# Kernel tuning notes

Measured on AMD Instinct MI355X. Metric: run time of the kernel, lower is better.

## Reference

```python
import jax, jax.numpy as jnp
import numpy as np

B, S, D_IN, D_OUT = 8, 2048, 1024, 1024

def setup_inputs() -> dict:
    key = jax.random.key(0)
    k1, k2, k3, k4 = jax.random.split(key, 4)
    sc = 0.02
    return {
        "x": jax.random.normal(k1, (B, S, D_IN), dtype=jnp.float32),
        "Wq": jax.random.normal(k2, (D_IN, D_OUT), dtype=jnp.float32) * sc,
        "Wk": jax.random.normal(k3, (D_IN, D_OUT), dtype=jnp.float32) * sc,
        "Wv": jax.random.normal(k4, (D_IN, D_OUT), dtype=jnp.float32) * sc,
    }

def reference(x, Wq, Wk, Wv):
    b, n, _ = x.shape
    d_out = Wq.shape[1]
    q = jnp.einsum('bsd,de->bse', x, Wq)   # [b, n, d_out]
    k = jnp.einsum('bsd,de->bse', x, Wk)
    v = jnp.einsum('bsd,de->bse', x, Wv)
    scores = jnp.einsum('bie,bje->bij', q, k)  # [b, n, n]
    # causal mask: positions j > i set to -inf (triu, diagonal=1)
    causal = jnp.triu(jnp.ones((n, n), dtype=bool), k=1)
    scores = jnp.where(causal[None, :, :], -jnp.inf, scores)
    # NOTE: source applies softmax over dim=1 (query axis), scaled by sqrt(d_out)
    weights = jax.nn.softmax(scores / jnp.sqrt(jnp.float32(d_out)), axis=1)
    # dropout is identity in eval mode (p=0)
    return jnp.einsum('bij,bje->bie', weights, v)
```

## Files before the change

kernel.cpp:

```cpp
#include <hip/hip_runtime.h>
#include <hip/hip_bf16.h>


using bf16 = __hip_bfloat16;
typedef __attribute__((ext_vector_type(8))) short short8;
typedef __attribute__((ext_vector_type(4))) float f32x4;

__device__ __forceinline__ float bfbits2f(unsigned short u) {
  return __uint_as_float((unsigned)u << 16);
}

__global__ void cvt_kernel(const float* __restrict__ in, bf16* __restrict__ out) {
  size_t i = ((size_t)blockIdx.x * 256 + threadIdx.x) * 4;
  float4 v = *(const float4*)(in + i);
  alignas(8) bf16 h[4] = {__float2bfloat16(v.x), __float2bfloat16(v.y),
                          __float2bfloat16(v.z), __float2bfloat16(v.w)};
  *(unsigned long long*)(out + i) = *(const unsigned long long*)h;
}

__global__ void pre_kernel(const float* __restrict__ x,
                           const float* __restrict__ W0, const float* __restrict__ W1,
                           const float* __restrict__ W2, bf16* __restrict__ Wt,
                           float* __restrict__ lbuf, bf16* __restrict__ Xb) {
  int tid = threadIdx.x;
  int zz = blockIdx.z;
  if (zz == 3) {
    int bid = blockIdx.y * 16 + blockIdx.x;
    if (bid < 64) lbuf[bid * 256 + tid] = 0.f;
    return;
  }
  if (zz >= 4) {
    size_t cb = (size_t)(zz - 4) * 256 + blockIdx.y * 16 + blockIdx.x;
    size_t i = (cb * 256 + tid) * 4;
    float4 v = *(const float4*)(x + i);
    alignas(8) bf16 h[4] = {__float2bfloat16(v.x), __float2bfloat16(v.y),
                            __float2bfloat16(v.z), __float2bfloat16(v.w)};
    *(unsigned long long*)(Xb + i) = *(const unsigned long long*)h;
    return;
  }
  const float* W = zz == 0 ? W0 : zz == 1 ? W1 : W2;
  bf16* O = Wt + (size_t)zz * 1048576ull;
  __shared__ float t[64][65];
  int n0 = blockIdx.x * 64, k0 = blockIdx.y * 64;
#pragma unroll
  for (int i = 0; i < 4; ++i) {
    int idx = i * 1024 + tid * 4;
    int r = idx >> 6, c = idx & 63;
    float4 v = *(const float4*)(W + (size_t)(k0 + r) * 1024 + n0 + c);
    t[r][c] = v.x; t[r][c + 1] = v.y; t[r][c + 2] = v.z; t[r][c + 3] = v.w;
  }
  __syncthreads();
#pragma unroll
  for (int i = 0; i < 4; ++i) {
    int idx = i * 1024 + tid * 4;
    int r = idx >> 6, c = idx & 63;
    alignas(8) bf16 h[4] = {__float2bfloat16(t[c][r]), __float2bfloat16(t[c + 1][r]),
                            __float2bfloat16(t[c + 2][r]), __float2bfloat16(t[c + 3][r])};
    *(unsigned long long*)(O + (size_t)(n0 + r) * 1024 + k0 + c) = *(const unsigned long long*)h;
  }
}

__global__ void vhat_kernel(const bf16* __restrict__ QKV, const float* __restrict__ l,
                            bf16* __restrict__ Vt) {
  int lb = blockIdx.z;
  const unsigned short* V =
      (const unsigned short*)QKV + ((size_t)lb * 3 + 2) * 2097152ull;
  bf16* O = Vt + (size_t)lb * 2097152ull;
  const float* lc = l + lb * 2048;
  __shared__ float t[64][65];
  __shared__ float rl[64];
  int j0 = blockIdx.x * 64, e0 = blockIdx.y * 64;
  int tid = threadIdx.x;
  if (tid < 64) rl[tid] = 1.0f / lc[j0 + tid];
#pragma unroll
  for (int i = 0; i < 4; ++i) {
    int idx = i * 1024 + tid * 4;
    int r = idx >> 6, c = idx & 63;
    ushort4 u = *(const ushort4*)(V + (size_t)(j0 + r) * 1024 + e0 + c);
    t[r][c] = bfbits2f(u.x); t[r][c + 1] = bfbits2f(u.y);
    t[r][c + 2] = bfbits2f(u.z); t[r][c + 3] = bfbits2f(u.w);
  }
  __syncthreads();
#pragma unroll
  for (int i = 0; i < 4; ++i) {
    int idx = i * 1024 + tid * 4;
    int r = idx >> 6, c = idx & 63;
    alignas(8) bf16 h[4] = {
        __float2bfloat16(t[c][r] * rl[c]), __float2bfloat16(t[c + 1][r] * rl[c + 1]),
        __float2bfloat16(t[c + 2][r] * rl[c + 2]), __float2bfloat16(t[c + 3][r] * rl[c + 3])};
    *(unsigned long long*)(O + (size_t)(e0 + r) * 2048 + j0 + c) = *(const unsigned long long*)h;
  }
}

template <int EPI, bool TRI>
__device__ __forceinline__ void gemm_bt_body(
    const bf16* __restrict__ A, const bf16* __restrict__ B, void* __restrict__ Cv,
    int lda, int ldb, int ldc, int Kin, int zdivA, int zmodB,
    unsigned long long sA, unsigned long long sB, unsigned long long sC,
    float* __restrict__ lptr) {
  unsigned bz, bx, by;
  if constexpr (TRI) {
    const unsigned gx = gridDim.x;
    const unsigned total = gx * gridDim.z;
    unsigned id = blockIdx.x + gx * blockIdx.z;
    unsigned lid = (id & 7) * (total >> 3) + (id >> 3);
    bz = lid / gx;
    unsigned t = lid - bz * gx;
    int r = (int)((__builtin_sqrtf(8.f * (float)t + 1.f) - 1.f) * 0.5f);
    while ((r + 1) * (r + 2) / 2 <= (int)t) ++r;
    while (r * (r + 1) / 2 > (int)t) --r;
    by = (unsigned)r;
    bx = t - (unsigned)(r * (r + 1) / 2);
  } else {
    const unsigned gx = gridDim.x, gy = gridDim.y;
    const unsigned per_z = gx * gy;
    const unsigned total = per_z * gridDim.z;
    unsigned id = blockIdx.x + gx * (blockIdx.y + gy * blockIdx.z);
    unsigned lid = (id & 7) * (total >> 3) + (id >> 3);
    bz = lid / per_z;
    unsigned rem = lid - bz * per_z;
    constexpr unsigned H = 8;
    const unsigned band = rem / (gx * H);
    const unsigned w = rem - band * (gx * H);
    bx = w / H;
    by = band * H + (w - bx * H);
  }

  const int z = (int)bz;
  A += (unsigned long long)(z / zdivA) * sA;
  B += (unsigned long long)(z % zmodB) * sB;
  const int K = Kin;

  alignas(16) __shared__ bf16 As[128 * 64];
  alignas(16) __shared__ bf16 Bs[128 * 64];

  const int tid = threadIdx.x, wave = tid >> 6, lane = tid & 63;
  const int m0 = by * 128, n0 = bx * 128;
  const int srow = tid >> 3;
  const int scol_g = ((tid & 7) ^ (srow & 7)) * 8;
  const int scol_l = (tid & 7) * 8;
  const int wm = (wave >> 1) * 64, wn = (wave & 1) * 64;
  const int fm = lane & 15, sw = lane & 7, kg = lane >> 4;

  f32x4 acc[4][4];
#pragma unroll
  for (int mi = 0; mi < 4; ++mi)
#pragma unroll
    for (int ni = 0; ni < 4; ++ni) acc[mi][ni] = (f32x4){0.f, 0.f, 0.f, 0.f};

  const bf16* Arow = A + (size_t)m0 * lda;
  const bf16* Brow = B + (size_t)n0 * ldb;

  for (int k0 = 0; k0 < K; k0 += 64) {
    __syncthreads();
#pragma unroll
    for (int c = 0; c < 4; ++c) {
      int row = c * 32 + srow;
      __builtin_amdgcn_global_load_lds(
          (const __attribute__((address_space(1))) void*)(Arow + (size_t)row * lda + k0 + scol_g),
          (__attribute__((address_space(3))) void*)(As + row * 64 + scol_l), 16, 0, 0);
    }
#pragma unroll
    for (int c = 0; c < 4; ++c) {
      int row = c * 32 + srow;
      __builtin_amdgcn_global_load_lds(
          (const __attribute__((address_space(1))) void*)(Brow + (size_t)row * ldb + k0 + scol_g),
          (__attribute__((address_space(3))) void*)(Bs + row * 64 + scol_l), 16, 0, 0);
    }
    __syncthreads();
#pragma unroll
    for (int ks = 0; ks < 2; ++ks) {
      const int pc = ((ks * 4 + kg) ^ sw) * 8;
      short8 af[4], bf_[4];
#pragma unroll
      for (int i = 0; i < 4; ++i) {
        af[i] = *(const short8*)(As + (wm + i * 16 + fm) * 64 + pc);
        bf_[i] = *(const short8*)(Bs + (wn + i * 16 + fm) * 64 + pc);
      }
#pragma unroll
      for (int mi = 0; mi < 4; ++mi)
#pragma unroll
        for (int ni = 0; ni < 4; ++ni)
          acc[mi][ni] = __builtin_amdgcn_mfma_f32_16x16x32_bf16(af[mi], bf_[ni], acc[mi][ni], 0, 0, 0);
    }
  }

  const int cr = kg * 4, cc = fm;
  if constexpr (EPI == 0) {
    bf16* C = (bf16*)Cv + (unsigned long long)z * sC;
#pragma unroll
    for (int mi = 0; mi < 4; ++mi)
#pragma unroll
      for (int ni = 0; ni < 4; ++ni)
#pragma unroll
        for (int r = 0; r < 4; ++r)
          C[(size_t)(m0 + wm + mi * 16 + cr + r) * ldc + (n0 + wn + ni * 16 + cc)] =
              __float2bfloat16(acc[mi][ni][r]);
  } else {
    bf16* C = (bf16*)Cv + (unsigned long long)z * sC;
    float colpart[4] = {0.f, 0.f, 0.f, 0.f};
#pragma unroll
    for (int mi = 0; mi < 4; ++mi)
#pragma unroll
      for (int ni = 0; ni < 4; ++ni)
#pragma unroll
        for (int r = 0; r < 4; ++r) {
          int gm = m0 + wm + mi * 16 + cr + r;
          int gn = n0 + wn + ni * 16 + cc;
          float s = acc[mi][ni][r] * 0.03125f;
          float p = (gn <= gm) ? __expf(s) : 0.f;
          colpart[ni] += p;
          C[(size_t)gm * ldc + gn] = __float2bfloat16(p);
        }
    float* lcol = lptr + (size_t)z * 2048 + n0 + wn;
#pragma unroll
    for (int ni = 0; ni < 4; ++ni) {
      float s = colpart[ni];
      s += __shfl_xor(s, 16);
      s += __shfl_xor(s, 32);
      if (lane < 16) atomicAdd(&lcol[ni * 16 + lane], s);
    }
  }
}

__global__ __launch_bounds__(256, 4) void gemm_qkv(
    const bf16* __restrict__ A, const bf16* __restrict__ B, void* __restrict__ Cv,
    int lda, int ldb, int ldc, int Kin, int zdivA, int zmodB,
    unsigned long long sA, unsigned long long sB, unsigned long long sC) {
  gemm_bt_body<0, false>(A, B, Cv, lda, ldb, ldc, Kin, zdivA, zmodB, sA, sB, sC, nullptr);
}
__global__ __launch_bounds__(256, 4) void gemm_scores(
    const bf16* __restrict__ A, const bf16* __restrict__ B, void* __restrict__ Cv,
    int lda, int ldb, int ldc, int Kin, int zdivA, int zmodB,
    unsigned long long sA, unsigned long long sB, unsigned long long sC,
    float* __restrict__ lptr) {
  gemm_bt_body<1, true>(A, B, Cv, lda, ldb, ldc, Kin, zdivA, zmodB, sA, sB, sC, lptr);
}

__global__ __launch_bounds__(256, 4) void gemm_pv(
    const bf16* __restrict__ Pm, const bf16* __restrict__ Vt, float* __restrict__ out,
    unsigned long long sA, unsigned long long sB, unsigned long long sC) {
  const unsigned gx = gridDim.x, gy = gridDim.y;
  const unsigned per_z = gx * gy;
  const unsigned total = per_z * gridDim.z;
  unsigned id = blockIdx.x + gx * (blockIdx.y + gy * blockIdx.z);
  unsigned lid = (id & 7) * (total >> 3) + (id >> 3);
  const unsigned bz = lid / per_z;
  unsigned rem = lid - bz * per_z;
  const unsigned bx = rem >> 3;
  const unsigned pp = rem & 7;
  const int z = (int)bz;

  const bf16* A = Pm + (unsigned long long)z * sA;
  const bf16* B = Vt + (unsigned long long)z * sB;
  float* C = out + (unsigned long long)z * sC;

  alignas(16) __shared__ bf16 As[128 * 64];
  alignas(16) __shared__ bf16 Bs[128 * 64];

  const int tid = threadIdx.x, wave = tid >> 6, lane = tid & 63;
  const int srow = tid >> 3;
  const int scol_g = ((tid & 7) ^ (srow & 7)) * 8;
  const int scol_l = (tid & 7) * 8;
  const int wm = (wave >> 1) * 64, wn = (wave & 1) * 64;
  const int fm = lane & 15, sw = lane & 7, kg = lane >> 4;
  const int n0 = (int)bx * 128;
  const bf16* Brow = B + (size_t)n0 * 2048;

  auto phase = [&](int by, int K) {
    const int m0 = by * 128;
    const bf16* Arow = A + (size_t)m0 * 2048;
    f32x4 acc[4][4];
#pragma unroll
    for (int mi = 0; mi < 4; ++mi)
#pragma unroll
      for (int ni = 0; ni < 4; ++ni) acc[mi][ni] = (f32x4){0.f, 0.f, 0.f, 0.f};

    for (int k0 = 0; k0 < K; k0 += 64) {
      __syncthreads();
#pragma unroll
      for (int c = 0; c < 4; ++c) {
        int row = c * 32 + srow;
        __builtin_amdgcn_global_load_lds(
            (const __attribute__((address_space(1))) void*)(Arow + (size_t)row * 2048 + k0 + scol_g),
            (__attribute__((address_space(3))) void*)(As + row * 64 + scol_l), 16, 0, 0);
      }
#pragma unroll
      for (int c = 0; c < 4; ++c) {
        int row = c * 32 + srow;
        __builtin_amdgcn_global_load_lds(
            (const __attribute__((address_space(1))) void*)(Brow + (size_t)row * 2048 + k0 + scol_g),
            (__attribute__((address_space(3))) void*)(Bs + row * 64 + scol_l), 16, 0, 0);
      }
      __syncthreads();
#pragma unroll
      for (int ks = 0; ks < 2; ++ks) {
        const int pc = ((ks * 4 + kg) ^ sw) * 8;
        short8 af[4], bf_[4];
#pragma unroll
        for (int i = 0; i < 4; ++i) {
          af[i] = *(const short8*)(As + (wm + i * 16 + fm) * 64 + pc);
          bf_[i] = *(const short8*)(Bs + (wn + i * 16 + fm) * 64 + pc);
        }
#pragma unroll
        for (int mi = 0; mi < 4; ++mi)
#pragma unroll
          for (int ni = 0; ni < 4; ++ni)
            acc[mi][ni] = __builtin_amdgcn_mfma_f32_16x16x32_bf16(af[mi], bf_[ni], acc[mi][ni], 0, 0, 0);
      }
    }
    const int cr = kg * 4, cc = fm;
#pragma unroll
    for (int mi = 0; mi < 4; ++mi)
#pragma unroll
      for (int ni = 0; ni < 4; ++ni)
#pragma unroll
        for (int r = 0; r < 4; ++r)
          C[(size_t)(m0 + wm + mi * 16 + cr + r) * 1024 + (n0 + wn + ni * 16 + cc)] =
              acc[mi][ni][r];
  };

  phase(15 - (int)pp, (16 - (int)pp) * 128);
  phase((int)pp, ((int)pp + 1) * 128);
}

extern "C" void kernel_launch(void* const* d_in, const int* in_sizes, int n_in,
                              void* d_out, int out_size, void* d_ws, size_t ws_size,
                              hipStream_t stream) {
  const float* x = (const float*)d_in[0];
  const float* Wq = (const float*)d_in[1];
  const float* Wk = (const float*)d_in[2];
  const float* Wv = (const float*)d_in[3];
  float* out = (float*)d_out;

  constexpr unsigned long long X_EL = 2048ull * 1024;
  constexpr unsigned long long QKV_EL = 3ull * X_EL;
  constexpr unsigned long long P_EL = 2048ull * 2048;
  constexpr unsigned long long VT_EL = 1024ull * 2048;
  constexpr unsigned long long WT_B = 3ull * 1024 * 1024 * 2;
  constexpr unsigned long long LB_B = 8ull * 2048 * 4;
  constexpr unsigned long long PER_B = 2 * (X_EL + QKV_EL + P_EL + VT_EL);

  size_t NB = 1;
  for (size_t nb : {(size_t)8, (size_t)4, (size_t)2})
    if (WT_B + LB_B + nb * PER_B <= ws_size) { NB = nb; break; }

  char* p = (char*)d_ws;
  bf16* Wt = (bf16*)p;   p += WT_B;
  float* lbuf = (float*)p; p += LB_B;
  bf16* Xb = (bf16*)p;   p += 2 * NB * X_EL;
  bf16* QKV = (bf16*)p;  p += 2 * NB * QKV_EL;
  bf16* P = (bf16*)p;    p += 2 * NB * P_EL;
  bf16* Vt = (bf16*)p;

  pre_kernel<<<dim3(16, 16, (unsigned)(4 + NB * 8)), 256, 0, stream>>>(
      x, Wq, Wk, Wv, Wt, lbuf, Xb);

  for (size_t b0 = 0; b0 < 8; b0 += NB) {
    if (b0)
      cvt_kernel<<<dim3((unsigned)(NB * 2048)), 256, 0, stream>>>(x + b0 * X_EL, Xb);
    gemm_qkv<<<dim3(8, 16, (unsigned)(NB * 3)), 256, 0, stream>>>(
        Xb, Wt, QKV, 1024, 1024, 1024, 1024, 3, 3, X_EL, 1048576ull, X_EL);
    gemm_scores<<<dim3(136, 1, (unsigned)NB), 256, 0, stream>>>(
        QKV, QKV + X_EL, P, 1024, 1024, 2048, 1024, 1, 1 << 30, QKV_EL, QKV_EL, P_EL,
        lbuf + b0 * 2048);
    vhat_kernel<<<dim3(32, 16, (unsigned)NB), 256, 0, stream>>>(QKV, lbuf + b0 * 2048, Vt);
    gemm_pv<<<dim3(8, 8, (unsigned)NB), 256, 0, stream>>>(
        P, Vt, out + b0 * X_EL, P_EL, VT_EL, X_EL);
  }
}
```

Baseline: 327.1 us.

## Split causal PV GEMM into equal K-chunks across blocks with atomic partial sums

The PV GEMM previously paired row-tiles (15-p, p) per block to balance the causal triangle. Now the triangle's 136 K-steps per column tile are split into 16 equal 17-step segments. Each block handles one segment, possibly crossing row-tile boundaries, and writes full tiles directly or partial tiles via float atomicAdd. This doubles the grid to improve occupancy and balance, but it adds a memset of the output and atomic traffic on partial tiles.

```diff
diff --git a/kernel.cpp b/kernel.cpp
--- a/kernel.cpp
+++ b/kernel.cpp
@@ -5,6 +5,7 @@
 using bf16 = __hip_bfloat16;
 typedef __attribute__((ext_vector_type(8))) short short8;
 typedef __attribute__((ext_vector_type(4))) float f32x4;
+typedef unsigned long long ull;
 
 __device__ __forceinline__ float bfbits2f(unsigned short u) {
   return __uint_as_float((unsigned)u << 16);
@@ -247,8 +248,8 @@
   unsigned lid = (id & 7) * (total >> 3) + (id >> 3);
   const unsigned bz = lid / per_z;
   unsigned rem = lid - bz * per_z;
-  const unsigned bx = rem >> 3;
-  const unsigned pp = rem & 7;
+  const unsigned bx = rem >> 4;
+  const unsigned q = rem & 15;
   const int z = (int)bz;
 
   const bf16* A = Pm + (unsigned long long)z * sA;
@@ -266,17 +267,29 @@
   const int fm = lane & 15, sw = lane & 7, kg = lane >> 4;
   const int n0 = (int)bx * 128;
   const bf16* Brow = B + (size_t)n0 * 2048;
-
-  auto phase = [&](int by, int K) {
+  const int cr = kg * 4, cc = fm;
+
+  const int s0 = (int)q * 17, s1 = s0 + 17;
+  int by = 0;
+  while ((by + 1) * (by + 2) <= s0) ++by;
+  int cur = s0;
+
+  while (cur < s1) {
+    const int Cprev = by * (by + 1);
+    const int Cend = (by + 1) * (by + 2);
+    const int b = s1 < Cend ? s1 : Cend;
+    const int kbeg = (cur - Cprev) * 64, kend = (b - Cprev) * 64;
+    const bool full = (cur == Cprev) && (b == Cend);
     const int m0 = by * 128;
     const bf16* Arow = A + (size_t)m0 * 2048;
+
     f32x4 acc[4][4];
 #pragma unroll
     for (int mi = 0; mi < 4; ++mi)
 #pragma unroll
       for (int ni = 0; ni < 4; ++ni) acc[mi][ni] = (f32x4){0.f, 0.f, 0.f, 0.f};
 
-    for (int k0 = 0; k0 < K; k0 += 64) {
+    for (int k0 = kbeg; k0 < kend; k0 += 64) {
       __syncthreads();
 #pragma unroll
       for (int c = 0; c < 4; ++c) {
@@ -309,19 +322,29 @@
             acc[mi][ni] = __builtin_amdgcn_mfma_f32_16x16x32_bf16(af[mi], bf_[ni], acc[mi][ni], 0, 0, 0);
       }
     }
-    const int cr = kg * 4, cc = fm;
-#pragma unroll
-    for (int mi = 0; mi < 4; ++mi)
-#pragma unroll
-      for (int ni = 0; ni < 4; ++ni)
-#pragma unroll
-        for (int r = 0; r < 4; ++r)
-          C[(size_t)(m0 + wm + mi * 16 + cr + r) * 1024 + (n0 + wn + ni * 16 + cc)] =
-              acc[mi][ni][r];
-  };
-
-  phase(15 - (int)pp, (16 - (int)pp) * 128);
-  phase((int)pp, ((int)pp + 1) * 128);
+
+    if (full) {
+#pragma unroll
+      for (int mi = 0; mi < 4; ++mi)
+#pragma unroll
+        for (int ni = 0; ni < 4; ++ni)
+#pragma unroll
+          for (int r = 0; r < 4; ++r)
+            C[(size_t)(m0 + wm + mi * 16 + cr + r) * 1024 + (n0 + wn + ni * 16 + cc)] =
+                acc[mi][ni][r];
+    } else {
+#pragma unroll
+      for (int mi = 0; mi < 4; ++mi)
+#pragma unroll
+        for (int ni = 0; ni < 4; ++ni)
+#pragma unroll
+          for (int r = 0; r < 4; ++r)
+            atomicAdd(&C[(size_t)(m0 + wm + mi * 16 + cr + r) * 1024 + (n0 + wn + ni * 16 + cc)],
+                      acc[mi][ni][r]);
+    }
+    cur = b;
+    ++by;
+  }
 }
 
 extern "C" void kernel_launch(void* const* d_in, const int* in_sizes, int n_in,
@@ -352,6 +375,8 @@
   bf16* QKV = (bf16*)p;  p += 2 * NB * QKV_EL;
   bf16* P = (bf16*)p;    p += 2 * NB * P_EL;
   bf16* Vt = (bf16*)p;
+
+  hipMemsetAsync(d_out, 0, (size_t)out_size, stream);
 
   pre_kernel<<<dim3(16, 16, (unsigned)(4 + NB * 8)), 256, 0, stream>>>(
       x, Wq, Wk, Wv, Wt, lbuf, Xb);
@@ -365,7 +390,7 @@
         QKV, QKV + X_EL, P, 1024, 1024, 2048, 1024, 1, 1 << 30, QKV_EL, QKV_EL, P_EL,
         lbuf + b0 * 2048);
     vhat_kernel<<<dim3(32, 16, (unsigned)NB), 256, 0, stream>>>(QKV, lbuf + b0 * 2048, Vt);
-    gemm_pv<<<dim3(8, 8, (unsigned)NB), 256, 0, stream>>>(
+    gemm_pv<<<dim3(16, 8, (unsigned)NB), 256, 0, stream>>>(
         P, Vt, out + b0 * X_EL, P_EL, VT_EL, X_EL);
   }
 }
```

Result: slower. 387.5 us (+18.4%).

## Fuse V-transpose-scale into PV GEMM via cooperative grid sync

Applied to the files above, without the earlier changes.

Merges the vhat transpose/normalize kernel into the PV GEMM kernel, using a grid-stride loop over the transpose tiles followed by a cooperative-groups grid-wide sync before the GEMM phase. The two kernels now share one shared-memory buffer. The aim is to remove one kernel launch and the gap between launches. In exchange it adds a cooperative launch with a grid barrier, and the transpose phase runs on only the PV grid's block count (64*NB), which may lower parallelism in that phase.

```diff
diff --git a/kernel.cpp b/kernel.cpp
--- a/kernel.cpp
+++ b/kernel.cpp
@@ -1,10 +1,14 @@
 #include <hip/hip_runtime.h>
 #include <hip/hip_bf16.h>
+#include <hip/hip_cooperative_groups.h>
+
+namespace cg = cooperative_groups;
 
 
 using bf16 = __hip_bfloat16;
 typedef __attribute__((ext_vector_type(8))) short short8;
 typedef __attribute__((ext_vector_type(4))) float f32x4;
+typedef unsigned long long ull;
 
 __device__ __forceinline__ float bfbits2f(unsigned short u) {
   return __uint_as_float((unsigned)u << 16);
@@ -57,38 +61,6 @@
     alignas(8) bf16 h[4] = {__float2bfloat16(t[c][r]), __float2bfloat16(t[c + 1][r]),
                             __float2bfloat16(t[c + 2][r]), __float2bfloat16(t[c + 3][r])};
     *(unsigned long long*)(O + (size_t)(n0 + r) * 1024 + k0 + c) = *(const unsigned long long*)h;
-  }
-}
-
-__global__ void vhat_kernel(const bf16* __restrict__ QKV, const float* __restrict__ l,
-                            bf16* __restrict__ Vt) {
-  int lb = blockIdx.z;
-  const unsigned short* V =
-      (const unsigned short*)QKV + ((size_t)lb * 3 + 2) * 2097152ull;
-  bf16* O = Vt + (size_t)lb * 2097152ull;
-  const float* lc = l + lb * 2048;
-  __shared__ float t[64][65];
-  __shared__ float rl[64];
-  int j0 = blockIdx.x * 64, e0 = blockIdx.y * 64;
-  int tid = threadIdx.x;
-  if (tid < 64) rl[tid] = 1.0f / lc[j0 + tid];
-#pragma unroll
-  for (int i = 0; i < 4; ++i) {
-    int idx = i * 1024 + tid * 4;
-    int r = idx >> 6, c = idx & 63;
-    ushort4 u = *(const ushort4*)(V + (size_t)(j0 + r) * 1024 + e0 + c);
-    t[r][c] = bfbits2f(u.x); t[r][c + 1] = bfbits2f(u.y);
-    t[r][c + 2] = bfbits2f(u.z); t[r][c + 3] = bfbits2f(u.w);
-  }
-  __syncthreads();
-#pragma unroll
-  for (int i = 0; i < 4; ++i) {
-    int idx = i * 1024 + tid * 4;
-    int r = idx >> 6, c = idx & 63;
-    alignas(8) bf16 h[4] = {
-        __float2bfloat16(t[c][r] * rl[c]), __float2bfloat16(t[c + 1][r] * rl[c + 1]),
-        __float2bfloat16(t[c + 2][r] * rl[c + 2]), __float2bfloat16(t[c + 3][r] * rl[c + 3])};
-    *(unsigned long long*)(O + (size_t)(e0 + r) * 2048 + j0 + c) = *(const unsigned long long*)h;
   }
 }
 
@@ -237,14 +209,59 @@
   gemm_bt_body<1, true>(A, B, Cv, lda, ldb, ldc, Kin, zdivA, zmodB, sA, sB, sC, lptr);
 }
 
-__global__ __launch_bounds__(256, 4) void gemm_pv(
-    const bf16* __restrict__ Pm, const bf16* __restrict__ Vt, float* __restrict__ out,
+__global__ __launch_bounds__(256, 4) void vhat_pv(
+    const bf16* __restrict__ QKV, const float* __restrict__ l, bf16* __restrict__ Vt,
+    const bf16* __restrict__ Pm, float* __restrict__ out,
     unsigned long long sA, unsigned long long sB, unsigned long long sC) {
+  alignas(16) __shared__ char smem[32768];
+  const int tid = threadIdx.x;
+  const unsigned nblk = gridDim.x * gridDim.y * gridDim.z;
+  const unsigned flat = blockIdx.x + gridDim.x * (blockIdx.y + gridDim.y * blockIdx.z);
+
+  {
+    float (*t)[65] = (float(*)[65])smem;
+    float* rl = (float*)(smem + 64 * 65 * 4);
+    const unsigned ntile = 512u * gridDim.z;
+    for (unsigned g = flat; g < ntile; g += nblk) {
+      const int lb = (int)(g >> 9);
+      const unsigned rem = g & 511;
+      const int j0 = (int)(rem >> 4) * 64;
+      const int e0 = (int)(rem & 15) * 64;
+      const unsigned short* V =
+          (const unsigned short*)QKV + ((size_t)lb * 3 + 2) * 2097152ull;
+      bf16* O = Vt + (size_t)lb * 2097152ull;
+      const float* lc = l + lb * 2048;
+      if (g != flat) __syncthreads();
+      if (tid < 64) rl[tid] = 1.0f / lc[j0 + tid];
+#pragma unroll
+      for (int i = 0; i < 4; ++i) {
+        int idx = i * 1024 + tid * 4;
+        int r = idx >> 6, c = idx & 63;
+        ushort4 u = *(const ushort4*)(V + (size_t)(j0 + r) * 1024 + e0 + c);
+        t[r][c] = bfbits2f(u.x); t[r][c + 1] = bfbits2f(u.y);
+        t[r][c + 2] = bfbits2f(u.z); t[r][c + 3] = bfbits2f(u.w);
+      }
+      __syncthreads();
+#pragma unroll
+      for (int i = 0; i < 4; ++i) {
+        int idx = i * 1024 + tid * 4;
+        int r = idx >> 6, c = idx & 63;
+        alignas(8) bf16 h[4] = {
+            __float2bfloat16(t[c][r] * rl[c]), __float2bfloat16(t[c + 1][r] * rl[c + 1]),
+            __float2bfloat16(t[c + 2][r] * rl[c + 2]), __float2bfloat16(t[c + 3][r] * rl[c + 3])};
+        *(unsigned long long*)(O + (size_t)(e0 + r) * 2048 + j0 + c) =
+            *(const unsigned long long*)h;
+      }
+    }
+  }
+  __threadfence();
+  cg::this_grid().sync();
+
+  bf16* As = (bf16*)smem;
+  bf16* Bs = (bf16*)(smem + 16384);
   const unsigned gx = gridDim.x, gy = gridDim.y;
   const unsigned per_z = gx * gy;
-  const unsigned total = per_z * gridDim.z;
-  unsigned id = blockIdx.x + gx * (blockIdx.y + gy * blockIdx.z);
-  unsigned lid = (id & 7) * (total >> 3) + (id >> 3);
+  unsigned lid = (flat & 7) * (nblk >> 3) + (flat >> 3);
   const unsigned bz = lid / per_z;
   unsigned rem = lid - bz * per_z;
   const unsigned bx = rem >> 3;
@@ -255,10 +272,7 @@
   const bf16* B = Vt + (unsigned long long)z * sB;
   float* C = out + (unsigned long long)z * sC;
 
-  alignas(16) __shared__ bf16 As[128 * 64];
-  alignas(16) __shared__ bf16 Bs[128 * 64];
-
-  const int tid = threadIdx.x, wave = tid >> 6, lane = tid & 63;
+  const int wave = tid >> 6, lane = tid & 63;
   const int srow = tid >> 3;
   const int scol_g = ((tid & 7) ^ (srow & 7)) * 8;
   const int scol_l = (tid & 7) * 8;
@@ -364,8 +378,17 @@
     gemm_scores<<<dim3(136, 1, (unsigned)NB), 256, 0, stream>>>(
         QKV, QKV + X_EL, P, 1024, 1024, 2048, 1024, 1, 1 << 30, QKV_EL, QKV_EL, P_EL,
         lbuf + b0 * 2048);
-    vhat_kernel<<<dim3(32, 16, (unsigned)NB), 256, 0, stream>>>(QKV, lbuf + b0 * 2048, Vt);
-    gemm_pv<<<dim3(8, 8, (unsigned)NB), 256, 0, stream>>>(
-        P, Vt, out + b0 * X_EL, P_EL, VT_EL, X_EL);
-  }
-}
+    {
+      const bf16* QKVa = QKV;
+      const float* la = lbuf + b0 * 2048;
+      bf16* Vta = Vt;
+      const bf16* Pa = P;
+      float* outa = out + b0 * X_EL;
+      unsigned long long sA = P_EL, sB = VT_EL, sC = X_EL;
+      void* args[] = {(void*)&QKVa, (void*)&la, (void*)&Vta, (void*)&Pa,
+                      (void*)&outa, (void*)&sA, (void*)&sB, (void*)&sC};
+      hipLaunchCooperativeKernel(reinterpret_cast<void*>(vhat_pv),
+                                 dim3(8, 8, (unsigned)NB), dim3(256), args, 0, stream);
+    }
+  }
+}
```

Measured after the change: 462.9 us. 1.41x slower.

## Fuse V scaling/transpose into scores GEMM via last-block-per-column counter

Applied to the files above, without the earlier changes.

Removes the separate vhat kernel. Each scores block increments a per-column-strip atomic counter, and the last block to finish a 128-column strip reads the completed column sums and writes the scaled, transposed V tile for that strip. This saves a launch and lets the V transposition overlap with the remaining GEMM tiles. It adds fence/atomic synchronisation and serial tail work in single blocks, which may lengthen the critical path.

```diff
diff --git a/kernel.cpp b/kernel.cpp
--- a/kernel.cpp
+++ b/kernel.cpp
@@ -5,6 +5,7 @@
 using bf16 = __hip_bfloat16;
 typedef __attribute__((ext_vector_type(8))) short short8;
 typedef __attribute__((ext_vector_type(4))) float f32x4;
+typedef unsigned long long ull;
 
 __device__ __forceinline__ float bfbits2f(unsigned short u) {
   return __uint_as_float((unsigned)u << 16);
@@ -21,12 +22,14 @@
 __global__ void pre_kernel(const float* __restrict__ x,
                            const float* __restrict__ W0, const float* __restrict__ W1,
                            const float* __restrict__ W2, bf16* __restrict__ Wt,
-                           float* __restrict__ lbuf, bf16* __restrict__ Xb) {
+                           float* __restrict__ lbuf, int* __restrict__ cnt,
+                           bf16* __restrict__ Xb) {
   int tid = threadIdx.x;
   int zz = blockIdx.z;
   if (zz == 3) {
     int bid = blockIdx.y * 16 + blockIdx.x;
     if (bid < 64) lbuf[bid * 256 + tid] = 0.f;
+    else if (bid == 64 && tid < 128) cnt[tid] = 0;
     return;
   }
   if (zz >= 4) {
@@ -60,44 +63,12 @@
   }
 }
 
-__global__ void vhat_kernel(const bf16* __restrict__ QKV, const float* __restrict__ l,
-                            bf16* __restrict__ Vt) {
-  int lb = blockIdx.z;
-  const unsigned short* V =
-      (const unsigned short*)QKV + ((size_t)lb * 3 + 2) * 2097152ull;
-  bf16* O = Vt + (size_t)lb * 2097152ull;
-  const float* lc = l + lb * 2048;
-  __shared__ float t[64][65];
-  __shared__ float rl[64];
-  int j0 = blockIdx.x * 64, e0 = blockIdx.y * 64;
-  int tid = threadIdx.x;
-  if (tid < 64) rl[tid] = 1.0f / lc[j0 + tid];
-#pragma unroll
-  for (int i = 0; i < 4; ++i) {
-    int idx = i * 1024 + tid * 4;
-    int r = idx >> 6, c = idx & 63;
-    ushort4 u = *(const ushort4*)(V + (size_t)(j0 + r) * 1024 + e0 + c);
-    t[r][c] = bfbits2f(u.x); t[r][c + 1] = bfbits2f(u.y);
-    t[r][c + 2] = bfbits2f(u.z); t[r][c + 3] = bfbits2f(u.w);
-  }
-  __syncthreads();
-#pragma unroll
-  for (int i = 0; i < 4; ++i) {
-    int idx = i * 1024 + tid * 4;
-    int r = idx >> 6, c = idx & 63;
-    alignas(8) bf16 h[4] = {
-        __float2bfloat16(t[c][r] * rl[c]), __float2bfloat16(t[c + 1][r] * rl[c + 1]),
-        __float2bfloat16(t[c + 2][r] * rl[c + 2]), __float2bfloat16(t[c + 3][r] * rl[c + 3])};
-    *(unsigned long long*)(O + (size_t)(e0 + r) * 2048 + j0 + c) = *(const unsigned long long*)h;
-  }
-}
-
 template <int EPI, bool TRI>
 __device__ __forceinline__ void gemm_bt_body(
     const bf16* __restrict__ A, const bf16* __restrict__ B, void* __restrict__ Cv,
     int lda, int ldb, int ldc, int Kin, int zdivA, int zmodB,
     unsigned long long sA, unsigned long long sB, unsigned long long sC,
-    float* __restrict__ lptr) {
+    float* __restrict__ lptr, int* __restrict__ cntp, bf16* __restrict__ vtp) {
   unsigned bz, bx, by;
   if constexpr (TRI) {
     const unsigned gx = gridDim.x;
@@ -131,8 +102,12 @@
   B += (unsigned long long)(z % zmodB) * sB;
   const int K = Kin;
 
-  alignas(16) __shared__ bf16 As[128 * 64];
-  alignas(16) __shared__ bf16 Bs[128 * 64];
+  __shared__ union SM {
+    struct { alignas(16) bf16 As[128 * 64]; alignas(16) bf16 Bs[128 * 64]; } g;
+    struct { float t[64][65]; float rl[128]; int done; } v;
+  } sm;
+  bf16* As = sm.g.As;
+  bf16* Bs = sm.g.Bs;
 
   const int tid = threadIdx.x, wave = tid >> 6, lane = tid & 63;
   const int m0 = by * 128, n0 = bx * 128;
@@ -220,6 +195,48 @@
       s += __shfl_xor(s, 32);
       if (lane < 16) atomicAdd(&lcol[ni * 16 + lane], s);
     }
+
+    __syncthreads();
+    if (tid == 0) {
+      __threadfence();
+      int old = atomicAdd(&cntp[z * 16 + (int)bx], 1);
+      sm.v.done = (old == 15 - (int)bx) ? 1 : 0;
+    }
+    __syncthreads();
+    if (!sm.v.done) return;
+    __threadfence();
+    if (tid < 128) {
+      float lv = atomicAdd(&lptr[(size_t)z * 2048 + (int)bx * 128 + tid], 0.0f);
+      sm.v.rl[tid] = 1.0f / lv;
+    }
+    const unsigned short* V = (const unsigned short*)A + 2ull * 2097152ull;
+    bf16* O = vtp + (size_t)z * 2097152ull;
+    for (int it = 0; it < 32; ++it) {
+      const int jb = it & 1, eb = it >> 1;
+      const int j0 = (int)bx * 128 + jb * 64, e0 = eb * 64;
+      __syncthreads();
+#pragma unroll
+      for (int i = 0; i < 4; ++i) {
+        int idx = i * 1024 + tid * 4;
+        int r = idx >> 6, c2 = idx & 63;
+        ushort4 u = *(const ushort4*)(V + (size_t)(j0 + r) * 1024 + e0 + c2);
+        sm.v.t[r][c2] = bfbits2f(u.x); sm.v.t[r][c2 + 1] = bfbits2f(u.y);
+        sm.v.t[r][c2 + 2] = bfbits2f(u.z); sm.v.t[r][c2 + 3] = bfbits2f(u.w);
+      }
+      __syncthreads();
+#pragma unroll
+      for (int i = 0; i < 4; ++i) {
+        int idx = i * 1024 + tid * 4;
+        int r = idx >> 6, c2 = idx & 63;
+        alignas(8) bf16 h[4] = {
+            __float2bfloat16(sm.v.t[c2][r] * sm.v.rl[jb * 64 + c2]),
+            __float2bfloat16(sm.v.t[c2 + 1][r] * sm.v.rl[jb * 64 + c2 + 1]),
+            __float2bfloat16(sm.v.t[c2 + 2][r] * sm.v.rl[jb * 64 + c2 + 2]),
+            __float2bfloat16(sm.v.t[c2 + 3][r] * sm.v.rl[jb * 64 + c2 + 3])};
+        *(unsigned long long*)(O + (size_t)(e0 + r) * 2048 + j0 + c2) =
+            *(const unsigned long long*)h;
+      }
+    }
   }
 }
 
@@ -227,14 +244,16 @@
     const bf16* __restrict__ A, const bf16* __restrict__ B, void* __restrict__ Cv,
     int lda, int ldb, int ldc, int Kin, int zdivA, int zmodB,
     unsigned long long sA, unsigned long long sB, unsigned long long sC) {
-  gemm_bt_body<0, false>(A, B, Cv, lda, ldb, ldc, Kin, zdivA, zmodB, sA, sB, sC, nullptr);
+  gemm_bt_body<0, false>(A, B, Cv, lda, ldb, ldc, Kin, zdivA, zmodB, sA, sB, sC,
+                         nullptr, nullptr, nullptr);
 }
 __global__ __launch_bounds__(256, 4) void gemm_scores(
     const bf16* __restrict__ A, const bf16* __restrict__ B, void* __restrict__ Cv,
     int lda, int ldb, int ldc, int Kin, int zdivA, int zmodB,
     unsigned long long sA, unsigned long long sB, unsigned long long sC,
-    float* __restrict__ lptr) {
-  gemm_bt_body<1, true>(A, B, Cv, lda, ldb, ldc, Kin, zdivA, zmodB, sA, sB, sC, lptr);
+    float* __restrict__ lptr, int* __restrict__ cntp, bf16* __restrict__ vtp) {
+  gemm_bt_body<1, true>(A, B, Cv, lda, ldb, ldc, Kin, zdivA, zmodB, sA, sB, sC,
+                        lptr, cntp, vtp);
 }
 
 __global__ __launch_bounds__(256, 4) void gemm_pv(
@@ -339,22 +358,24 @@
   constexpr unsigned long long VT_EL = 1024ull * 2048;
   constexpr unsigned long long WT_B = 3ull * 1024 * 1024 * 2;
   constexpr unsigned long long LB_B = 8ull * 2048 * 4;
+  constexpr unsigned long long CNT_B = 512;
   constexpr unsigned long long PER_B = 2 * (X_EL + QKV_EL + P_EL + VT_EL);
 
   size_t NB = 1;
   for (size_t nb : {(size_t)8, (size_t)4, (size_t)2})
-    if (WT_B + LB_B + nb * PER_B <= ws_size) { NB = nb; break; }
+    if (WT_B + LB_B + CNT_B + nb * PER_B <= ws_size) { NB = nb; break; }
 
   char* p = (char*)d_ws;
   bf16* Wt = (bf16*)p;   p += WT_B;
   float* lbuf = (float*)p; p += LB_B;
+  int* cnt = (int*)p;    p += CNT_B;
   bf16* Xb = (bf16*)p;   p += 2 * NB * X_EL;
   bf16* QKV = (bf16*)p;  p += 2 * NB * QKV_EL;
   bf16* P = (bf16*)p;    p += 2 * NB * P_EL;
   bf16* Vt = (bf16*)p;
 
   pre_kernel<<<dim3(16, 16, (unsigned)(4 + NB * 8)), 256, 0, stream>>>(
-      x, Wq, Wk, Wv, Wt, lbuf, Xb);
+      x, Wq, Wk, Wv, Wt, lbuf, cnt, Xb);
 
   for (size_t b0 = 0; b0 < 8; b0 += NB) {
     if (b0)
@@ -363,8 +384,7 @@
         Xb, Wt, QKV, 1024, 1024, 1024, 1024, 3, 3, X_EL, 1048576ull, X_EL);
     gemm_scores<<<dim3(136, 1, (unsigned)NB), 256, 0, stream>>>(
         QKV, QKV + X_EL, P, 1024, 1024, 2048, 1024, 1, 1 << 30, QKV_EL, QKV_EL, P_EL,
-        lbuf + b0 * 2048);
-    vhat_kernel<<<dim3(32, 16, (unsigned)NB), 256, 0, stream>>>(QKV, lbuf + b0 * 2048, Vt);
+        lbuf + b0 * 2048, cnt + b0 * 16, Vt);
     gemm_pv<<<dim3(8, 8, (unsigned)NB), 256, 0, stream>>>(
         P, Vt, out + b0 * X_EL, P_EL, VT_EL, X_EL);
   }
```

Measured after the change: 428.8 us. +31.1%, slower.
